# Optimization experiments

Measured on AMD Instinct MI355X. Metric: run time of the kernel, lower is better.

Reference implementation:

```python
import jax, jax.numpy as jnp
import numpy as np

B, S, M = 4, 4096, 2048
LATENT, H, D = 512, 16, 128  # latent_dim, num_heads, hidden_dim (per-head)


def setup_inputs() -> dict:
    key = jax.random.key(0)
    ks = jax.random.split(key, 12)
    sd = lambda fan_in: 1.0 / np.sqrt(fan_in)
    return {
        "x": jax.random.normal(ks[0], (B, S, M), dtype=jnp.float32),
        # k path: down-proj to latent, up-proj to H*D (vmapped Dense pair, slice 0)
        "Wd_k": jax.random.normal(ks[1], (M, LATENT), dtype=jnp.float32) * sd(M),
        "bd_k": jnp.zeros((LATENT,), dtype=jnp.float32),
        "Wu_k": jax.random.normal(ks[2], (LATENT, H * D), dtype=jnp.float32) * sd(LATENT),
        "bu_k": jnp.zeros((H * D,), dtype=jnp.float32),
        # v path (slice 1 of the vmapped params)
        "Wd_v": jax.random.normal(ks[3], (M, LATENT), dtype=jnp.float32) * sd(M),
        "bd_v": jnp.zeros((LATENT,), dtype=jnp.float32),
        "Wu_v": jax.random.normal(ks[4], (LATENT, H * D), dtype=jnp.float32) * sd(LATENT),
        "bu_v": jnp.zeros((H * D,), dtype=jnp.float32),
        # q projection
        "Wq": jax.random.normal(ks[5], (M, H * D), dtype=jnp.float32) * sd(M),
        "bq": jnp.zeros((H * D,), dtype=jnp.float32),
        # output projection
        "Wo": jax.random.normal(ks[6], (H * D, M), dtype=jnp.float32) * sd(H * D),
        "bo": jnp.zeros((M,), dtype=jnp.float32),
    }


def reference(x, Wd_k, bd_k, Wu_k, bu_k, Wd_v, bd_v, Wu_v, bu_v, Wq, bq, Wo, bo):
    b, s, m = x.shape
    # low-rank KV: down-project to latent cache, up-project to heads
    cache_k = x @ Wd_k + bd_k                      # [B,S,L]
    cache_v = x @ Wd_v + bd_v                      # [B,S,L]
    k = (cache_k @ Wu_k + bu_k).reshape(b, s, H, D)
    v = (cache_v @ Wu_v + bu_v).reshape(b, s, H, D)
    q = (x @ Wq + bq).reshape(b, s, H, D)
    # NOTE: source permutes k as (0,1,3,2) on [B,S,H,D] -> scores are per-token
    # head-vs-head [B,S,H,H], softmax over the last (head) axis.
    sim = jnp.einsum("bshd,bsgd->bshg", q, k) * (D ** -0.5)
    attn = jax.nn.softmax(sim, axis=-1)            # [B,S,H,H]
    out = jnp.einsum("bshg,bsgd->bshd", attn, v)   # [B,S,H,D]
    out = out.reshape(b, s, H * D)
    return out @ Wo + bo                           # [B,S,M]
```

## Files before the change

### kernel.cpp

```cpp
#include <hip/hip_runtime.h>

typedef __attribute__((ext_vector_type(8))) short short8v;
typedef __attribute__((ext_vector_type(4))) float f32x4;
typedef __attribute__((ext_vector_type(4))) unsigned int uint4v;

#define GLOBAL_AS(p) ((const __attribute__((address_space(1))) void*)(p))
#define LDS_AS(p)    ((__attribute__((address_space(3))) void*)(p))
#define WAITV(n) asm volatile("s_waitcnt vmcnt(" #n ")" ::: "memory")
#define BARRIER() __builtin_amdgcn_s_barrier()

__device__ __forceinline__ unsigned short f2bf(float f) {
  unsigned int u = __builtin_bit_cast(unsigned int, f);
  u += 0x7fffu + ((u >> 16) & 1u);
  return (unsigned short)(u >> 16);
}
__device__ __forceinline__ float bf2f(unsigned short u) {
  unsigned int x = ((unsigned int)u) << 16;
  return __builtin_bit_cast(float, x);
}

__global__ __launch_bounds__(256) void transpose_to_bf16(
    const float* __restrict__ src, unsigned short* __restrict__ dst,
    int K, int N, int ntx) {
  __shared__ float tile[32][33];
  const int bx = blockIdx.x % ntx;
  const int by = blockIdx.x / ntx;
  const int tx = threadIdx.x & 31, ty = threadIdx.x >> 5;
  const int k0 = by * 32, n0 = bx * 32;
#pragma unroll
  for (int i = 0; i < 32; i += 8)
    tile[ty + i][tx] = src[(size_t)(k0 + ty + i) * N + n0 + tx];
  __syncthreads();
#pragma unroll
  for (int i = 0; i < 32; i += 8)
    dst[(size_t)(n0 + ty + i) * K + k0 + tx] = f2bf(tile[tx][ty + i]);
}

__global__ __launch_bounds__(256) void cvt_f32_bf16(
    const float* __restrict__ s, unsigned short* __restrict__ d) {
  const int o = blockIdx.x;
  const size_t row = (size_t)((o & 7) * 2048 + (o >> 3));
  size_t i = row * 2048 + threadIdx.x * 8;
  f32x4 v0 = *(const f32x4*)(s + i);
  f32x4 v1 = *(const f32x4*)(s + i + 4);
  union U8 { uint4v v; unsigned short us[8]; } o8;
  o8.us[0] = f2bf(v0.x); o8.us[1] = f2bf(v0.y); o8.us[2] = f2bf(v0.z); o8.us[3] = f2bf(v0.w);
  o8.us[4] = f2bf(v1.x); o8.us[5] = f2bf(v1.y); o8.us[6] = f2bf(v1.z); o8.us[7] = f2bf(v1.w);
  *(uint4v*)(d + i) = o8.v;
}

__global__ __launch_bounds__(256) void fill_bias(
    const float* __restrict__ bd_k, const float* __restrict__ bd_v,
    const float* __restrict__ bq, const float* __restrict__ bu_k,
    const float* __restrict__ bu_v, float* __restrict__ b1, float* __restrict__ b2) {
  int i = blockIdx.x * 256 + threadIdx.x;
  if (i < 512) b1[i] = bd_k[i];
  else if (i < 1024) b1[i] = bd_v[i - 512];
  else if (i < 3072) b1[i] = bq[i - 1024];
  else if (i < 5120) b2[i - 3072] = bu_k[i - 3072];
  else if (i < 7168) b2[i - 3072] = bu_v[i - 5120];
}

template <int OUT_BF16>
__global__ __launch_bounds__(256, 2) void gemm_bt(
    const unsigned short* __restrict__ A, int lda, int nsplit_col, int acol_off,
    const unsigned short* __restrict__ Bt, int ldb,
    const float* __restrict__ bias, void* __restrict__ Cp, int ldc,
    int K, int ntn) {
  __shared__ unsigned short Als[256 * 64];
  __shared__ unsigned short Bls[128 * 64];
  const int t = threadIdx.x;
  const int lane = t & 63, wave = t >> 6;

  const int qx = gridDim.x >> 3;
  const int bid = (blockIdx.x & 7) * qx + (blockIdx.x >> 3);
  const int bm = (bid / ntn) * 256;
  const int bn = (bid % ntn) * 128;
  const unsigned short* Ab = A + (bn >= nsplit_col ? acol_off : 0);

  const int wr = wave >> 1, wc = wave & 1;
  const int g = lane >> 4, r = lane & 15;
  const int swz = r & 7;
  const int NT = K >> 6;

  f32x4 acc[8][4];
#pragma unroll
  for (int i = 0; i < 8; ++i)
#pragma unroll
    for (int j = 0; j < 4; ++j) acc[i][j] = (f32x4){0.f, 0.f, 0.f, 0.f};

  const int srow = t >> 3;
  const int jsrc = (t & 7) ^ (srow & 7);
  const unsigned short* aptr = Ab + (size_t)(bm + srow) * lda + (jsrc << 3);
  const unsigned short* bptr = Bt + (size_t)(bn + srow) * ldb + (jsrc << 3);
  const int wbase = wave * 512;

  for (int T = 0; T < NT; ++T) {
    const unsigned short* ak = aptr + (size_t)T * 64;
    const unsigned short* bk = bptr + (size_t)T * 64;
#pragma unroll
    for (int u = 0; u < 8; ++u)
      __builtin_amdgcn_global_load_lds(GLOBAL_AS(ak + (size_t)(u * 32) * lda),
                                       LDS_AS(&Als[u * 2048 + wbase]), 16, 0, 0);
#pragma unroll
    for (int u = 0; u < 4; ++u)
      __builtin_amdgcn_global_load_lds(GLOBAL_AS(bk + (size_t)(u * 32) * ldb),
                                       LDS_AS(&Bls[u * 2048 + wbase]), 16, 0, 0);
    WAITV(0);
    BARRIER();
#pragma unroll
    for (int ks = 0; ks < 2; ++ks) {
      const int c16 = (((ks << 2) + g) ^ swz) << 3;
      short8v bf[4];
#pragma unroll
      for (int ni = 0; ni < 4; ++ni)
        bf[ni] = *(const short8v*)&Bls[(wc * 64 + ni * 16 + r) * 64 + c16];
      __builtin_amdgcn_s_setprio(1);
#pragma unroll
      for (int mi = 0; mi < 8; ++mi) {
        short8v af = *(const short8v*)&Als[(wr * 128 + mi * 16 + r) * 64 + c16];
#pragma unroll
        for (int ni = 0; ni < 4; ++ni)
          acc[mi][ni] = __builtin_amdgcn_mfma_f32_16x16x32_bf16(
              af, bf[ni], acc[mi][ni], 0, 0, 0);
      }
      __builtin_amdgcn_s_setprio(0);
    }
    BARRIER();
  }

#pragma unroll
  for (int ni = 0; ni < 4; ++ni) {
    const int col = bn + wc * 64 + ni * 16 + r;
    const float bv = bias[col];
#pragma unroll
    for (int mi = 0; mi < 8; ++mi) {
      const int row0 = bm + wr * 128 + mi * 16 + (g << 2);
#pragma unroll
      for (int j = 0; j < 4; ++j) {
        float v = acc[mi][ni][j] + bv;
        if (OUT_BF16)
          ((unsigned short*)Cp)[(size_t)(row0 + j) * ldc + col] = f2bf(v);
        else
          ((float*)Cp)[(size_t)(row0 + j) * ldc + col] = v;
      }
    }
  }
}

__global__ __launch_bounds__(256) void attn_kernel(
    const unsigned short* __restrict__ out1, const unsigned short* __restrict__ kv,
    unsigned short* __restrict__ aout) {
  const int o = blockIdx.x;
  const int s = (o & 7) * 2048 + (o >> 3);
  const int t = threadIdx.x;
  __shared__ float qs[16 * 132], ks2[16 * 132], vs[16 * 132];
  __shared__ float attn[256];
  const int h = t >> 4, d0 = (t & 15) * 8;

  union U8 { uint4v v; unsigned short us[8]; };
  U8 qv, kv8, vv;
  qv.v = *(const uint4v*)(out1 + (size_t)s * 3072 + 1024 + t * 8);
  kv8.v = *(const uint4v*)(kv + (size_t)s * 4096 + t * 8);
  vv.v = *(const uint4v*)(kv + (size_t)s * 4096 + 2048 + t * 8);
#pragma unroll
  for (int j = 0; j < 8; ++j) {
    qs[h * 132 + d0 + j] = bf2f(qv.us[j]);
    ks2[h * 132 + d0 + j] = bf2f(kv8.us[j]);
    vs[h * 132 + d0 + j] = bf2f(vv.us[j]);
  }
  __syncthreads();

  const int gg0 = t & 15;
  const f32x4* qrow = (const f32x4*)&qs[h * 132];
  const f32x4* krow = (const f32x4*)&ks2[gg0 * 132];
  float acc = 0.f;
#pragma unroll
  for (int dd = 0; dd < 32; ++dd) {
    f32x4 a4 = qrow[dd], b4 = krow[dd];
    acc += a4.x * b4.x + a4.y * b4.y + a4.z * b4.z + a4.w * b4.w;
  }
  acc *= 0.08838834764831845f;
  float mx = acc;
#pragma unroll
  for (int ofs = 8; ofs; ofs >>= 1) mx = fmaxf(mx, __shfl_xor(mx, ofs));
  float e = __expf(acc - mx);
  float sm = e;
#pragma unroll
  for (int ofs = 8; ofs; ofs >>= 1) sm += __shfl_xor(sm, ofs);
  attn[t] = e / sm;
  __syncthreads();

  f32x4 o0 = (f32x4){0.f, 0.f, 0.f, 0.f}, o1 = (f32x4){0.f, 0.f, 0.f, 0.f};
#pragma unroll
  for (int gg = 0; gg < 16; ++gg) {
    const float a = attn[(h << 4) + gg];
    f32x4 v0 = *(const f32x4*)&vs[gg * 132 + d0];
    f32x4 v1 = *(const f32x4*)&vs[gg * 132 + d0 + 4];
    o0 += v0 * a;
    o1 += v1 * a;
  }
  U8 ov;
  ov.us[0] = f2bf(o0.x); ov.us[1] = f2bf(o0.y); ov.us[2] = f2bf(o0.z); ov.us[3] = f2bf(o0.w);
  ov.us[4] = f2bf(o1.x); ov.us[5] = f2bf(o1.y); ov.us[6] = f2bf(o1.z); ov.us[7] = f2bf(o1.w);
  *(uint4v*)(aout + (size_t)s * 2048 + t * 8) = ov.v;
}

extern "C" void kernel_launch(void* const* d_in, const int* in_sizes, int n_in,
                              void* d_out, int out_size, void* d_ws, size_t ws_size,
                              hipStream_t stream) {
  (void)in_sizes; (void)n_in; (void)out_size; (void)ws_size;
  const float* x    = (const float*)d_in[0];
  const float* Wd_k = (const float*)d_in[1];
  const float* bd_k = (const float*)d_in[2];
  const float* Wu_k = (const float*)d_in[3];
  const float* bu_k = (const float*)d_in[4];
  const float* Wd_v = (const float*)d_in[5];
  const float* bd_v = (const float*)d_in[6];
  const float* Wu_v = (const float*)d_in[7];
  const float* bu_v = (const float*)d_in[8];
  const float* Wq   = (const float*)d_in[9];
  const float* bq   = (const float*)d_in[10];
  const float* Wo   = (const float*)d_in[11];
  const float* bo   = (const float*)d_in[12];

  char* ws = (char*)d_ws;
  unsigned short* w1t  = (unsigned short*)(ws);
  unsigned short* w2t  = (unsigned short*)(ws + 12582912);
  unsigned short* w3t  = (unsigned short*)(ws + 16777216);
  float*          b1   = (float*)(ws + 25165824);
  float*          b2   = (float*)(ws + 25178112);
  unsigned short* xb   = (unsigned short*)(ws + 25194496);
  unsigned short* out1 = (unsigned short*)(ws + 92303360);
  unsigned short* kvb  = (unsigned short*)(ws + 192966656);
  unsigned short* attO = xb;

  dim3 blk(256);

  transpose_to_bf16<<<dim3(16 * 64), blk, 0, stream>>>(Wd_k, w1t,               2048, 512, 16);
  transpose_to_bf16<<<dim3(16 * 64), blk, 0, stream>>>(Wd_v, w1t + 512 * 2048,  2048, 512, 16);
  transpose_to_bf16<<<dim3(64 * 64), blk, 0, stream>>>(Wq,   w1t + 1024 * 2048, 2048, 2048, 64);
  transpose_to_bf16<<<dim3(64 * 16), blk, 0, stream>>>(Wu_k, w2t,               512, 2048, 64);
  transpose_to_bf16<<<dim3(64 * 16), blk, 0, stream>>>(Wu_v, w2t + 2048 * 512,  512, 2048, 64);
  transpose_to_bf16<<<dim3(64 * 64), blk, 0, stream>>>(Wo,   w3t,               2048, 2048, 64);

  fill_bias<<<dim3(28), blk, 0, stream>>>(bd_k, bd_v, bq, bu_k, bu_v, b1, b2);

  cvt_f32_bf16<<<dim3(16384), blk, 0, stream>>>(x, xb);

  gemm_bt<1><<<dim3(64 * 24), blk, 0, stream>>>(
      xb, 2048, 1 << 30, 0, w1t, 2048, b1, out1, 3072, 2048, 24);

  gemm_bt<1><<<dim3(64 * 32), blk, 0, stream>>>(
      out1, 3072, 2048, 512, w2t, 512, b2, kvb, 4096, 512, 32);

  attn_kernel<<<dim3(16384), blk, 0, stream>>>(out1, kvb, attO);

  gemm_bt<0><<<dim3(64 * 16), blk, 0, stream>>>(
      attO, 2048, 1 << 30, 0, w3t, 2048, bo, (float*)d_out, 2048, 2048, 16);
}
```

Before: 580.9 us.

## Double-buffer GEMM LDS tiles and enlarge block tile to 256x256

The bf16 GEMM kernel now uses a 256x256 output tile per block, up from 256x128, with 8x8 MFMA accumulators per wave. It double-buffers the LDS A/B tiles, so global-to-LDS loads for the next K step overlap the MFMA work on the current one. Occupancy drops to one block per CU because of the large register and LDS footprint, and the grids shrink to match (for example 512 blocks for the output projection). The aim is more data reuse per load and hidden load latency, at the cost of fewer blocks to schedule and possible register pressure.

New measurement: 687.8 us. 18.4% more time.

```diff
diff --git a/kernel.cpp b/kernel.cpp
--- a/kernel.cpp
+++ b/kernel.cpp
@@ -62,32 +62,31 @@
 }
 
 template <int OUT_BF16>
-__global__ __launch_bounds__(256, 2) void gemm_bt(
+__global__ __launch_bounds__(256, 1) void gemm_bt(
     const unsigned short* __restrict__ A, int lda, int nsplit_col, int acol_off,
     const unsigned short* __restrict__ Bt, int ldb,
     const float* __restrict__ bias, void* __restrict__ Cp, int ldc,
     int K, int ntn) {
-  __shared__ unsigned short Als[256 * 64];
-  __shared__ unsigned short Bls[128 * 64];
+  __shared__ unsigned short Als[2][256 * 64];
+  __shared__ unsigned short Bls[2][256 * 64];
   const int t = threadIdx.x;
   const int lane = t & 63, wave = t >> 6;
 
   const int qx = gridDim.x >> 3;
   const int bid = (blockIdx.x & 7) * qx + (blockIdx.x >> 3);
   const int bm = (bid / ntn) * 256;
-  const int bn = (bid % ntn) * 128;
+  const int bn = (bid % ntn) * 256;
   const unsigned short* Ab = A + (bn >= nsplit_col ? acol_off : 0);
 
   const int wr = wave >> 1, wc = wave & 1;
   const int g = lane >> 4, r = lane & 15;
-  const int swz = r & 7;
   const int NT = K >> 6;
 
-  f32x4 acc[8][4];
+  f32x4 acc[8][8];
 #pragma unroll
   for (int i = 0; i < 8; ++i)
 #pragma unroll
-    for (int j = 0; j < 4; ++j) acc[i][j] = (f32x4){0.f, 0.f, 0.f, 0.f};
+    for (int j = 0; j < 8; ++j) acc[i][j] = (f32x4){0.f, 0.f, 0.f, 0.f};
 
   const int srow = t >> 3;
   const int jsrc = (t & 7) ^ (srow & 7);
@@ -95,43 +94,64 @@
   const unsigned short* bptr = Bt + (size_t)(bn + srow) * ldb + (jsrc << 3);
   const int wbase = wave * 512;
 
+  auto stage = [&](int kt, int buf) {
+    const unsigned short* ak = aptr + (size_t)kt * 64;
+    const unsigned short* bk = bptr + (size_t)kt * 64;
+#pragma unroll
+    for (int u = 0; u < 8; ++u) {
+      __builtin_amdgcn_global_load_lds(GLOBAL_AS(ak + (size_t)(u * 32) * lda),
+                                       LDS_AS(&Als[buf][u * 2048 + wbase]), 16, 0, 0);
+      __builtin_amdgcn_global_load_lds(GLOBAL_AS(bk + (size_t)(u * 32) * ldb),
+                                       LDS_AS(&Bls[buf][u * 2048 + wbase]), 16, 0, 0);
+    }
+  };
+
+  stage(0, 0);
+
   for (int T = 0; T < NT; ++T) {
-    const unsigned short* ak = aptr + (size_t)T * 64;
-    const unsigned short* bk = bptr + (size_t)T * 64;
-#pragma unroll
-    for (int u = 0; u < 8; ++u)
-      __builtin_amdgcn_global_load_lds(GLOBAL_AS(ak + (size_t)(u * 32) * lda),
-                                       LDS_AS(&Als[u * 2048 + wbase]), 16, 0, 0);
-#pragma unroll
-    for (int u = 0; u < 4; ++u)
-      __builtin_amdgcn_global_load_lds(GLOBAL_AS(bk + (size_t)(u * 32) * ldb),
-                                       LDS_AS(&Bls[u * 2048 + wbase]), 16, 0, 0);
-    WAITV(0);
+    const int cur = T & 1;
+    if (T + 1 < NT) {
+      stage(T + 1, cur ^ 1);
+      WAITV(16);
+    } else {
+      WAITV(0);
+    }
     BARRIER();
-#pragma unroll
-    for (int ks = 0; ks < 2; ++ks) {
-      const int c16 = (((ks << 2) + g) ^ swz) << 3;
-      short8v bf[4];
-#pragma unroll
-      for (int ni = 0; ni < 4; ++ni)
-        bf[ni] = *(const short8v*)&Bls[(wc * 64 + ni * 16 + r) * 64 + c16];
-      __builtin_amdgcn_s_setprio(1);
-#pragma unroll
-      for (int mi = 0; mi < 8; ++mi) {
-        short8v af = *(const short8v*)&Als[(wr * 128 + mi * 16 + r) * 64 + c16];
-#pragma unroll
-        for (int ni = 0; ni < 4; ++ni)
-          acc[mi][ni] = __builtin_amdgcn_mfma_f32_16x16x32_bf16(
-              af, bf[ni], acc[mi][ni], 0, 0, 0);
-      }
-      __builtin_amdgcn_s_setprio(0);
-    }
+    const unsigned short* la = Als[cur];
+    const unsigned short* lb = Bls[cur];
+    const int c0 = (g ^ (r & 7)) << 3;
+    const int c1 = ((4 + g) ^ (r & 7)) << 3;
+    short8v a0[8], b0[8], a1[8], b1[8];
+#pragma unroll
+    for (int i = 0; i < 8; ++i) {
+      a0[i] = *(const short8v*)&la[(wr * 128 + i * 16 + r) * 64 + c0];
+      b0[i] = *(const short8v*)&lb[(wc * 128 + i * 16 + r) * 64 + c0];
+    }
+#pragma unroll
+    for (int i = 0; i < 8; ++i) {
+      a1[i] = *(const short8v*)&la[(wr * 128 + i * 16 + r) * 64 + c1];
+      b1[i] = *(const short8v*)&lb[(wc * 128 + i * 16 + r) * 64 + c1];
+    }
+    __builtin_amdgcn_s_setprio(1);
+#pragma unroll
+    for (int mi = 0; mi < 8; ++mi)
+#pragma unroll
+      for (int ni = 0; ni < 8; ++ni)
+        acc[mi][ni] = __builtin_amdgcn_mfma_f32_16x16x32_bf16(
+            a0[mi], b0[ni], acc[mi][ni], 0, 0, 0);
+#pragma unroll
+    for (int mi = 0; mi < 8; ++mi)
+#pragma unroll
+      for (int ni = 0; ni < 8; ++ni)
+        acc[mi][ni] = __builtin_amdgcn_mfma_f32_16x16x32_bf16(
+            a1[mi], b1[ni], acc[mi][ni], 0, 0, 0);
+    __builtin_amdgcn_s_setprio(0);
     BARRIER();
   }
 
 #pragma unroll
-  for (int ni = 0; ni < 4; ++ni) {
-    const int col = bn + wc * 64 + ni * 16 + r;
+  for (int ni = 0; ni < 8; ++ni) {
+    const int col = bn + wc * 128 + ni * 16 + r;
     const float bv = bias[col];
 #pragma unroll
     for (int mi = 0; mi < 8; ++mi) {
@@ -248,14 +268,14 @@
 
   cvt_f32_bf16<<<dim3(16384), blk, 0, stream>>>(x, xb);
 
-  gemm_bt<1><<<dim3(64 * 24), blk, 0, stream>>>(
-      xb, 2048, 1 << 30, 0, w1t, 2048, b1, out1, 3072, 2048, 24);
-
-  gemm_bt<1><<<dim3(64 * 32), blk, 0, stream>>>(
-      out1, 3072, 2048, 512, w2t, 512, b2, kvb, 4096, 512, 32);
+  gemm_bt<1><<<dim3(64 * 12), blk, 0, stream>>>(
+      xb, 2048, 1 << 30, 0, w1t, 2048, b1, out1, 3072, 2048, 12);
+
+  gemm_bt<1><<<dim3(64 * 16), blk, 0, stream>>>(
+      out1, 3072, 2048, 512, w2t, 512, b2, kvb, 4096, 512, 16);
 
   attn_kernel<<<dim3(16384), blk, 0, stream>>>(out1, kvb, attO);
 
-  gemm_bt<0><<<dim3(64 * 16), blk, 0, stream>>>(
-      attO, 2048, 1 << 30, 0, w3t, 2048, bo, (float*)d_out, 2048, 2048, 16);
-}
+  gemm_bt<0><<<dim3(64 * 8), blk, 0, stream>>>(
+      attO, 2048, 1 << 30, 0, w3t, 2048, bo, (float*)d_out, 2048, 2048, 8);
+}
```

## Double-buffer A tile in GEMM and merge weight transposes into one launch

Applied to the files above, without the earlier changes.

The GEMM now keeps two A-tile LDS buffers and issues global-to-LDS loads for the next B tile and the A tile two steps ahead. It waits with a partial vmcnt, so memory loads overlap the MFMA work instead of stalling on every tile. The six weight-transpose launches are merged into a single kernel that picks its matrix from the block index, saving launch overhead. LDS use per block grows from 48KB to 80KB, which may cut occupancy below the two-blocks-per-CU launch bound.

Result: no change. 571.7 us (-1.6%).

```diff
diff --git a/kernel.cpp b/kernel.cpp
--- a/kernel.cpp
+++ b/kernel.cpp
@@ -19,12 +19,22 @@
   return __builtin_bit_cast(float, x);
 }
 
-__global__ __launch_bounds__(256) void transpose_to_bf16(
-    const float* __restrict__ src, unsigned short* __restrict__ dst,
-    int K, int N, int ntx) {
+__global__ __launch_bounds__(256) void transpose_all(
+    const float* __restrict__ Wq, const float* __restrict__ Wo,
+    const float* __restrict__ Wd_k, const float* __restrict__ Wd_v,
+    const float* __restrict__ Wu_k, const float* __restrict__ Wu_v,
+    unsigned short* __restrict__ w1t, unsigned short* __restrict__ w2t,
+    unsigned short* __restrict__ w3t) {
+  int b = blockIdx.x;
+  const float* src; unsigned short* dst; int K, N, ntx;
+  if (b < 4096)      { src = Wq;   dst = w1t + 1024 * 2048; K = 2048; N = 2048; ntx = 64; }
+  else if (b < 8192) { src = Wo;   dst = w3t;               K = 2048; N = 2048; ntx = 64; b -= 4096; }
+  else if (b < 9216) { src = Wd_k; dst = w1t;               K = 2048; N = 512;  ntx = 16; b -= 8192; }
+  else if (b < 10240){ src = Wd_v; dst = w1t + 512 * 2048;  K = 2048; N = 512;  ntx = 16; b -= 9216; }
+  else if (b < 11264){ src = Wu_k; dst = w2t;               K = 512;  N = 2048; ntx = 64; b -= 10240; }
+  else               { src = Wu_v; dst = w2t + 2048 * 512;  K = 512;  N = 2048; ntx = 64; b -= 11264; }
   __shared__ float tile[32][33];
-  const int bx = blockIdx.x % ntx;
-  const int by = blockIdx.x / ntx;
+  const int bx = b % ntx, by = b / ntx;
   const int tx = threadIdx.x & 31, ty = threadIdx.x >> 5;
   const int k0 = by * 32, n0 = bx * 32;
 #pragma unroll
@@ -67,7 +77,7 @@
     const unsigned short* __restrict__ Bt, int ldb,
     const float* __restrict__ bias, void* __restrict__ Cp, int ldc,
     int K, int ntn) {
-  __shared__ unsigned short Als[256 * 64];
+  __shared__ unsigned short Als[2][256 * 64];
   __shared__ unsigned short Bls[128 * 64];
   const int t = threadIdx.x;
   const int lane = t & 63, wave = t >> 6;
@@ -95,19 +105,29 @@
   const unsigned short* bptr = Bt + (size_t)(bn + srow) * ldb + (jsrc << 3);
   const int wbase = wave * 512;
 
-  for (int T = 0; T < NT; ++T) {
-    const unsigned short* ak = aptr + (size_t)T * 64;
-    const unsigned short* bk = bptr + (size_t)T * 64;
+  auto stageA = [&](int kt, int buf) {
+    const unsigned short* ak = aptr + (size_t)kt * 64;
 #pragma unroll
     for (int u = 0; u < 8; ++u)
       __builtin_amdgcn_global_load_lds(GLOBAL_AS(ak + (size_t)(u * 32) * lda),
-                                       LDS_AS(&Als[u * 2048 + wbase]), 16, 0, 0);
+                                       LDS_AS(&Als[buf][u * 2048 + wbase]), 16, 0, 0);
+  };
+  auto stageB = [&](int kt) {
+    const unsigned short* bk = bptr + (size_t)kt * 64;
 #pragma unroll
     for (int u = 0; u < 4; ++u)
       __builtin_amdgcn_global_load_lds(GLOBAL_AS(bk + (size_t)(u * 32) * ldb),
                                        LDS_AS(&Bls[u * 2048 + wbase]), 16, 0, 0);
-    WAITV(0);
+  };
+
+  stageA(0, 0);
+  stageB(0);
+  if (NT > 1) stageA(1, 1);
+
+  for (int T = 0; T < NT; ++T) {
+    if (T + 1 < NT) { WAITV(8); } else { WAITV(0); }
     BARRIER();
+    const unsigned short* la = Als[T & 1];
 #pragma unroll
     for (int ks = 0; ks < 2; ++ks) {
       const int c16 = (((ks << 2) + g) ^ swz) << 3;
@@ -118,7 +138,7 @@
       __builtin_amdgcn_s_setprio(1);
 #pragma unroll
       for (int mi = 0; mi < 8; ++mi) {
-        short8v af = *(const short8v*)&Als[(wr * 128 + mi * 16 + r) * 64 + c16];
+        short8v af = *(const short8v*)&la[(wr * 128 + mi * 16 + r) * 64 + c16];
 #pragma unroll
         for (int ni = 0; ni < 4; ++ni)
           acc[mi][ni] = __builtin_amdgcn_mfma_f32_16x16x32_bf16(
@@ -127,6 +147,10 @@
       __builtin_amdgcn_s_setprio(0);
     }
     BARRIER();
+    if (T + 1 < NT) {
+      stageB(T + 1);
+      if (T + 2 < NT) stageA(T + 2, T & 1);
+    }
   }
 
 #pragma unroll
@@ -237,13 +261,8 @@
 
   dim3 blk(256);
 
-  transpose_to_bf16<<<dim3(16 * 64), blk, 0, stream>>>(Wd_k, w1t,               2048, 512, 16);
-  transpose_to_bf16<<<dim3(16 * 64), blk, 0, stream>>>(Wd_v, w1t + 512 * 2048,  2048, 512, 16);
-  transpose_to_bf16<<<dim3(64 * 64), blk, 0, stream>>>(Wq,   w1t + 1024 * 2048, 2048, 2048, 64);
-  transpose_to_bf16<<<dim3(64 * 16), blk, 0, stream>>>(Wu_k, w2t,               512, 2048, 64);
-  transpose_to_bf16<<<dim3(64 * 16), blk, 0, stream>>>(Wu_v, w2t + 2048 * 512,  512, 2048, 64);
-  transpose_to_bf16<<<dim3(64 * 64), blk, 0, stream>>>(Wo,   w3t,               2048, 2048, 64);
-
+  transpose_all<<<dim3(12288), blk, 0, stream>>>(Wq, Wo, Wd_k, Wd_v, Wu_k, Wu_v,
+                                                 w1t, w2t, w3t);
   fill_bias<<<dim3(28), blk, 0, stream>>>(bd_k, bd_v, bq, bu_k, bu_v, b1, b2);
 
   cvt_f32_bf16<<<dim3(16384), blk, 0, stream>>>(x, xb);
```
